# Kernel tuning notes

Measured on AMD Instinct MI355X. Metric: run time of the kernel, lower is better.

Reference implementation:

```python
import jax, jax.numpy as jnp
import numpy as np
from jax import lax

B = 512          # scoring batch size
NC = 10          # n_classes
N_LAB = 256      # int(B * plb), plb = 0.5 (labeled indices are the first N_LAB)
TOL = 1e-3       # gtg_t
MAX_ITER = 30    # gtg_i
INTERM = 128
CH = [64, 128, 256, 512]
SZ = [32, 16, 8, 4]
EMB = 512


def setup_inputs() -> dict:
    key = jax.random.key(0)
    ks = jax.random.split(key, 16)
    inp = {}
    for i, (c, s) in enumerate(zip(CH, SZ)):
        inp["feat%d" % i] = jax.random.normal(ks[i], (B, c, s, s), jnp.float32)
        inp["conv_w%d" % i] = jax.random.normal(ks[4 + i], (c, c, 3, 3), jnp.float32) * 0.05
        inp["conv_b%d" % i] = jnp.zeros((c,), jnp.float32)
        inp["bn_g%d" % i] = jnp.ones((c,), jnp.float32)
        inp["bn_b%d" % i] = jnp.zeros((c,), jnp.float32)
        inp["lin_w%d" % i] = jax.random.normal(ks[8 + i], (INTERM, c), jnp.float32) * 0.05
        inp["lin_b%d" % i] = jnp.zeros((INTERM,), jnp.float32)
    inp["fin_w"] = jax.random.normal(ks[12], (1, 4 * INTERM), jnp.float32) * 0.05
    inp["fin_b"] = jnp.zeros((1,), jnp.float32)
    inp["embedds"] = jax.random.normal(ks[13], (B, EMB), jnp.float32)
    inp["labels"] = jax.random.randint(ks[14], (B,), 0, NC)
    return inp


def _branch(x, cw, cb, g, b, lw, lb):
    # Conv3x3(same) -> BatchNorm (train mode, batch stats, eps=1e-5) -> ReLU -> GAP -> Linear -> ReLU
    y = lax.conv_general_dilated(x, cw, (1, 1), 'SAME',
                                 dimension_numbers=('NCHW', 'OIHW', 'NCHW')) + cb[None, :, None, None]
    m = y.mean(axis=(0, 2, 3), keepdims=True)
    v = ((y - m) ** 2).mean(axis=(0, 2, 3), keepdims=True)  # biased variance (train-mode BN)
    y = jax.nn.relu(g[None, :, None, None] * (y - m) * lax.rsqrt(v + 1e-5) + b[None, :, None, None])
    y = y.mean(axis=(2, 3))  # AvgPool2d(feature_size) == global average pool -> [B, C]
    return jax.nn.relu(y @ lw.T + lb)


def _gtg(E, labels):
    # get_A_e_d: pairwise euclidean distances clamped to [0.1, 1.0]
    sq = jnp.sum(E * E, axis=1)
    d2 = jnp.maximum(sq[:, None] + sq[None, :] - 2.0 * (E @ E.T), 0.0)
    A0 = jnp.clip(jnp.sqrt(d2), 0.1, 1.0)
    # rbf kernel: 7th nearest neighbor (ascending for 'e_d') gives per-sample sigma
    seventh = E[jnp.argsort(A0, axis=1)[:, 6]]
    sig = jnp.clip(jnp.sqrt(jnp.sum((E - seventh) ** 2, axis=1)), 0.1, 1.0)
    A = jnp.clip(jnp.exp(-(A0 ** 2) / (sig[:, None] * sig[None, :])), 0.0, 1.0)
    # threshold strategy 'mean' with AM_function == 'e_d': A = where(A > mean(A), 1, A)
    A = jnp.where(A > A.mean(), 1.0, A)
    # AM_strategy 'mixed' with 'e_d': flip only the labeled x labeled block
    A = A.at[:N_LAB, :N_LAB].set(1.0 - A[:N_LAB, :N_LAB])
    # get_X: one-hot for labeled (first N_LAB), uniform 1/NC for unlabeled
    X0 = jnp.concatenate([jax.nn.one_hot(labels[:N_LAB], NC, dtype=jnp.float32),
                          jnp.full((B - N_LAB, NC), 1.0 / NC, jnp.float32)], axis=0)
    hist0 = jnp.zeros((B, MAX_ITER), jnp.float32)

    def cond(c):
        return (c[3] > TOL) & (c[2] < MAX_ITER)

    def body(c):
        X, h, i, _ = c
        Xn = X * (A @ X)
        Xn = Xn / jnp.sum(Xn, axis=1, keepdims=True)
        ent = -jnp.sum(jnp.where(Xn > 0, Xn * jnp.log(Xn), 0.0), axis=1)
        h = lax.dynamic_update_slice(h, ent[:, None], (0, i))
        return (Xn, h, i + 1, jnp.linalg.norm(Xn - X))

    X, h, _, _ = lax.while_loop(cond, body, (X0, hist0, jnp.int32(0), jnp.float32(jnp.inf)))
    return h.mean(axis=1), X  # ent_strategy == 'mean'


def reference(feat0, feat1, feat2, feat3,
              conv_w0, conv_b0, bn_g0, bn_b0, lin_w0, lin_b0,
              conv_w1, conv_b1, bn_g1, bn_b1, lin_w1, lin_b1,
              conv_w2, conv_b2, bn_g2, bn_b2, lin_w2, lin_b2,
              conv_w3, conv_b3, bn_g3, bn_b3, lin_w3, lin_b3,
              fin_w, fin_b, embedds, labels):
    o0 = _branch(feat0, conv_w0, conv_b0, bn_g0, bn_b0, lin_w0, lin_b0)
    o1 = _branch(feat1, conv_w1, conv_b1, bn_g1, bn_b1, lin_w1, lin_b1)
    o2 = _branch(feat2, conv_w2, conv_b2, bn_g2, bn_b2, lin_w2, lin_b2)
    o3 = _branch(feat3, conv_w3, conv_b3, bn_g3, bn_b3, lin_w3, lin_b3)
    y_pred = (jnp.concatenate([o0, o1, o2, o3], axis=1) @ fin_w.T + fin_b)[:, 0]
    y_true, X = _gtg(embedds, labels)
    labeled_mask = jnp.arange(B) < N_LAB
    return (y_pred, y_true, X, labeled_mask)
```

## Files before the change

kernel.cpp:

```cpp
#include <hip/hip_runtime.h>
#include <hip/hip_bf16.h>
#include <math.h>

static constexpr int kNC = 10;
static constexpr int kNLab = 256;
static constexpr int kMaxIter = 30;

using short8 = __attribute__((ext_vector_type(8))) short;
using f32x4  = __attribute__((ext_vector_type(4))) float;

__device__ __forceinline__ unsigned short f2bf(float f) {
  unsigned int u = __float_as_uint(f);
  u += 0x7FFFu + ((u >> 16) & 1u);
  return (unsigned short)(u >> 16);
}
__device__ __forceinline__ float bf2f(unsigned short u) {
  return __uint_as_float(((unsigned int)u) << 16);
}

template <int C, int S>
__global__ __launch_bounds__(256) void xpack_kernel(const float* __restrict__ x,
                                                    unsigned short* __restrict__ xp) {
  __shared__ float t[C][S + 1];
  const int n = blockIdx.x / S, h = blockIdx.x % S;
  const float* src = x + (size_t)n * C * S * S;
  for (int e = threadIdx.x; e < C * S; e += 256) {
    int c = e / S, w = e % S;
    t[c][w] = src[((size_t)c * S + h) * S + w];
  }
  __syncthreads();
  unsigned short* dst = xp + ((size_t)(n * S + h) * S) * C;
  for (int e = threadIdx.x; e < C * S; e += 256) {
    int w = e / C, c = e % C;
    dst[(size_t)w * C + c] = f2bf(t[c][w]);
  }
}

template <int C>
__global__ void wpack_kernel(const float* __restrict__ w, unsigned short* __restrict__ wpk) {
  constexpr int CO16T = C / 16, CIK = C / 32;
  int idx = blockIdx.x * 256 + threadIdx.x;
  if (idx >= 9 * C * C) return;
  int e = idx & 7, l = (idx >> 3) & 63;
  int rest = idx >> 9;
  int co16 = rest % CO16T;
  int rest2 = rest / CO16T;
  int cik = rest2 % CIK, tap = rest2 / CIK;
  int co = co16 * 16 + (l & 15);
  int ci = cik * 32 + (l >> 4) * 8 + e;
  wpk[idx] = f2bf(w[((size_t)co * C + ci) * 9 + tap]);
}

template <int C, int S, int NI, int NR, int WV, int MODE>
__global__ __launch_bounds__(WV * 64)
void conv_mfma(const unsigned short* __restrict__ xp, const unsigned short* __restrict__ wpk,
               const float* __restrict__ bias, unsigned short* __restrict__ y,
               float* __restrict__ psum, float* __restrict__ psq, int npart, int partBase,
               const float* __restrict__ scale, const float* __restrict__ shift,
               float* __restrict__ pp, int pxGlobalBase) {
  constexpr int SS = S * S;
  constexpr int PXT = WV * 64;
  constexpr int HR = NR + 2, HC = S + 2;
  constexpr int CIK = C / 32, CO16T = C / 16;
  constexpr int UNITS = NI * HR * HC * 4;
  static_assert(NI * NR * S == PXT, "tile mismatch");
  __shared__ __align__(16) char xs[NI * HR * HC * 80];

  const int tid = threadIdx.x;
  const int wv = tid >> 6, l = tid & 63, l15 = l & 15, l4 = l >> 4;
  const int coblk = blockIdx.y;
  const int co_base = coblk * 64;
  const int pxb = blockIdx.x * PXT;
  const int n_t = pxb / SS;
  const int r0 = (pxb % SS) / S;

  int pxoff[4];
#pragma unroll
  for (int bf = 0; bf < 4; ++bf) {
    int pxloc = wv * 64 + bf * 16 + l15;
    int ii = pxloc / (NR * S);
    int rr = (pxloc % (NR * S)) / S;
    int cc = pxloc % S;
    pxoff[bf] = ((ii * HR + rr) * HC + cc) * 80 + l4 * 16;
  }

  f32x4 acc[4][4];
#pragma unroll
  for (int a = 0; a < 4; ++a)
#pragma unroll
    for (int b = 0; b < 4; ++b) acc[a][b] = (f32x4){0.f, 0.f, 0.f, 0.f};

  for (int cik = 0; cik < CIK; ++cik) {
    __syncthreads();
    for (int u = tid; u < UNITS; u += PXT) {
      int k16 = u & 3;
      int t = u >> 2;
      int hc = t % HC;
      int t2 = t / HC;
      int hr = t2 % HR;
      int ii = t2 / HR;
      int row = r0 + hr - 1, col = hc - 1;
      uint4 v = {0u, 0u, 0u, 0u};
      if (row >= 0 && row < S && col >= 0 && col < S)
        v = *(const uint4*)(xp + ((size_t)((n_t + ii) * S + row) * S + col) * C + cik * 32 + k16 * 8);
      *(uint4*)(xs + t * 80 + k16 * 16) = v;
    }
    __syncthreads();
#pragma unroll
    for (int tap = 0; tap < 9; ++tap) {
      const int tapoff = ((tap / 3) * HC + (tap % 3)) * 80;
      short8 wf[4], xf[4];
#pragma unroll
      for (int af = 0; af < 4; ++af)
        wf[af] = *(const short8*)(wpk + ((size_t)((tap * CIK + cik) * CO16T + coblk * 4 + af) * 64 + l) * 8);
#pragma unroll
      for (int bf = 0; bf < 4; ++bf)
        xf[bf] = *(const short8*)(xs + pxoff[bf] + tapoff);
#pragma unroll
      for (int af = 0; af < 4; ++af)
#pragma unroll
        for (int bf = 0; bf < 4; ++bf)
          acc[af][bf] = __builtin_amdgcn_mfma_f32_16x16x32_bf16(wf[af], xf[bf], acc[af][bf], 0, 0, 0);
    }
  }

#pragma unroll
  for (int af = 0; af < 4; ++af) {
    const int co0 = co_base + af * 16 + l4 * 4;
    float4 bv = *(const float4*)(bias + co0);
    float s[4] = {0.f, 0.f, 0.f, 0.f}, q[4] = {0.f, 0.f, 0.f, 0.f};
    float4 sc4, sh4;
    if (MODE == 2) {
      sc4 = *(const float4*)(scale + co0);
      sh4 = *(const float4*)(shift + co0);
    }
#pragma unroll
    for (int bf = 0; bf < 4; ++bf) {
      float o[4];
#pragma unroll
      for (int r = 0; r < 4; ++r) o[r] = acc[af][bf][r] + ((const float*)&bv)[r];
      if (MODE == 0) {
        ushort4 pk;
        pk.x = f2bf(o[0]); pk.y = f2bf(o[1]); pk.z = f2bf(o[2]); pk.w = f2bf(o[3]);
        size_t px = (size_t)(pxb + wv * 64 + bf * 16 + l15);
        *(ushort4*)(y + px * C + co0) = pk;
      }
      if (MODE == 2) {
#pragma unroll
        for (int r = 0; r < 4; ++r)
          s[r] += fmaxf(fmaf(((const float*)&sc4)[r], o[r], ((const float*)&sh4)[r]), 0.f);
      } else {
#pragma unroll
        for (int r = 0; r < 4; ++r) { s[r] += o[r]; q[r] += o[r] * o[r]; }
      }
    }
#pragma unroll
    for (int m = 1; m < 16; m <<= 1) {
#pragma unroll
      for (int r = 0; r < 4; ++r) {
        s[r] += __shfl_xor(s[r], m);
        if (MODE != 2) q[r] += __shfl_xor(q[r], m);
      }
    }
    if (l15 == 0) {
      if (MODE == 2) {
        int n = (pxGlobalBase + pxb) / SS;
        int qw = ((pxGlobalBase + pxb) % SS) / 64 + wv;
#pragma unroll
        for (int r = 0; r < 4; ++r)
          pp[((size_t)(n * C + co0 + r)) * 16 + qw] = s[r];
      } else {
        int part = partBase + blockIdx.x * WV + wv;
#pragma unroll
        for (int r = 0; r < 4; ++r) {
          psum[(size_t)(co0 + r) * npart + part] = s[r];
          psq[(size_t)(co0 + r) * npart + part] = q[r];
        }
      }
    }
  }
}

__global__ __launch_bounds__(256)
void stats2_kernel(const float* __restrict__ psum, const float* __restrict__ psq,
                   const float* __restrict__ g, const float* __restrict__ bb,
                   float* __restrict__ scale, float* __restrict__ shift,
                   int npart, float invN) {
  int c = blockIdx.x;
  __shared__ float rs[256], rq[256];
  float s = 0.f, q = 0.f;
  for (int p = threadIdx.x; p < npart; p += 256) {
    s += psum[(size_t)c * npart + p];
    q += psq[(size_t)c * npart + p];
  }
  rs[threadIdx.x] = s; rq[threadIdx.x] = q;
  __syncthreads();
  for (int st = 128; st; st >>= 1) {
    if (threadIdx.x < st) { rs[threadIdx.x] += rs[threadIdx.x + st]; rq[threadIdx.x] += rq[threadIdx.x + st]; }
    __syncthreads();
  }
  if (threadIdx.x == 0) {
    float m = rs[0] * invN;
    float v = rq[0] * invN - m * m;
    float sc = g[c] / sqrtf(v + 1e-5f);
    scale[c] = sc;
    shift[c] = bb[c] - m * sc;
  }
}

template <int C, int S>
__global__ __launch_bounds__(256)
void pool_nhwc(const unsigned short* __restrict__ y, const float* __restrict__ scale,
               const float* __restrict__ shift, float* __restrict__ pooled) {
  constexpr int SS = S * S;
  int n = blockIdx.x;
  const unsigned short* yr = y + (size_t)n * SS * C;
  if (C >= 256) {
    for (int co = threadIdx.x; co < C; co += 256) {
      float sc = scale[co], sh = shift[co], s = 0.f;
      for (int p = 0; p < SS; ++p) s += fmaxf(fmaf(sc, bf2f(yr[(size_t)p * C + co]), sh), 0.f);
      pooled[(size_t)n * C + co] = s * (1.f / SS);
    }
  } else {
    constexpr int G = 256 / C;
    int co = threadIdx.x % C;
    int sl = threadIdx.x / C;
    float sc = scale[co], sh = shift[co], s = 0.f;
    for (int p = sl; p < SS; p += G) s += fmaxf(fmaf(sc, bf2f(yr[(size_t)p * C + co]), sh), 0.f);
    __shared__ float red[256];
    red[threadIdx.x] = s;
    __syncthreads();
    if (threadIdx.x < C) {
      float t = 0.f;
      for (int gg = 0; gg < G; ++gg) t += red[gg * C + co];
      pooled[(size_t)n * C + co] = t * (1.f / SS);
    }
  }
}

__global__ void poolfin_kernel(const float* __restrict__ pp, float* __restrict__ pooled) {
  int i = blockIdx.x * 256 + threadIdx.x;
  if (i >= 512 * 64) return;
  float s = 0.f;
  for (int qn = 0; qn < 16; ++qn) s += pp[(size_t)i * 16 + qn];
  pooled[i] = s * (1.f / 1024.f);
}

__global__ void lin_kernel(const float* __restrict__ pooled, const float* __restrict__ lw,
                           const float* __restrict__ lb, float* __restrict__ oc,
                           int C, int brOff) {
  int idx = blockIdx.x * 256 + threadIdx.x;
  if (idx >= 512 * 128) return;
  int j = idx & 127, n = idx >> 7;
  const float4* pr = (const float4*)(pooled + (size_t)n * C);
  const float4* wr = (const float4*)(lw + (size_t)j * C);
  float s = 0.f;
  for (int t = 0; t < C / 4; ++t) {
    float4 a = pr[t], b = wr[t];
    s += a.x * b.x + a.y * b.y + a.z * b.z + a.w * b.w;
  }
  s += lb[j];
  oc[n * 512 + brOff + j] = fmaxf(s, 0.f);
}

__global__ void ypred_kernel(const float* __restrict__ oc, const float* __restrict__ fw,
                             const float* __restrict__ fb, float* __restrict__ out) {
  int wv = threadIdx.x >> 6, l = threadIdx.x & 63;
  int n = blockIdx.x * 4 + wv;
  float s = 0.f;
  for (int k = l; k < 512; k += 64) s += oc[n * 512 + k] * fw[k];
#pragma unroll
  for (int m = 32; m; m >>= 1) s += __shfl_down(s, m);
  if (l == 0) out[n] = s + fb[0];
}

__global__ void sqnorm_kernel(const float* __restrict__ E, float* __restrict__ sq) {
  int wv = threadIdx.x >> 6, l = threadIdx.x & 63;
  int n = blockIdx.x * 4 + wv;
  const float* row = E + (size_t)n * 512;
  float s = 0.f;
  for (int k = l; k < 512; k += 64) { float v = row[k]; s += v * v; }
#pragma unroll
  for (int m = 32; m; m >>= 1) s += __shfl_down(s, m);
  if (l == 0) sq[n] = s;
}

__global__ __launch_bounds__(256) void a0_kernel(const float* __restrict__ E,
                                                 const float* __restrict__ sq,
                                                 float* __restrict__ A0) {
  int bi = blockIdx.x / 32, bj = blockIdx.x % 32;
  int ti = threadIdx.x % 16, tj = threadIdx.x / 16;
  __shared__ float Ei[16][68], Ej[16][68];
  float acc = 0.f;
  for (int k0 = 0; k0 < 512; k0 += 64) {
    for (int e = threadIdx.x; e < 1024; e += 256) {
      int rr = e >> 6, cc = e & 63;
      Ei[rr][cc] = E[(size_t)(bi * 16 + rr) * 512 + k0 + cc];
      Ej[rr][cc] = E[(size_t)(bj * 16 + rr) * 512 + k0 + cc];
    }
    __syncthreads();
#pragma unroll 16
    for (int kk = 0; kk < 64; ++kk) acc = fmaf(Ei[tj][kk], Ej[ti][kk], acc);
    __syncthreads();
  }
  int i = bi * 16 + tj, j = bj * 16 + ti;
  float d2 = fmaxf(sq[i] + sq[j] - 2.f * acc, 0.f);
  A0[(size_t)i * 512 + j] = fminf(fmaxf(sqrtf(d2), 0.1f), 1.0f);
}

__global__ void seventh_kernel(const float* __restrict__ A0, int* __restrict__ idx7) {
  int i = blockIdx.x * 256 + threadIdx.x;
  if (i >= 512) return;
  float v[7]; int ix[7];
#pragma unroll
  for (int t = 0; t < 7; ++t) { v[t] = 3.4e38f; ix[t] = 0; }
  const float* row = A0 + (size_t)i * 512;
  for (int j = 0; j < 512; ++j) {
    float a = row[j];
    if (a < v[6]) {
      int pos = 6;
      while (pos > 0 && a < v[pos - 1]) { v[pos] = v[pos - 1]; ix[pos] = ix[pos - 1]; --pos; }
      v[pos] = a; ix[pos] = j;
    }
  }
  idx7[i] = ix[6];
}

__global__ void sig_kernel(const float* __restrict__ E, const int* __restrict__ idx7,
                           float* __restrict__ sig) {
  int wv = threadIdx.x >> 6, l = threadIdx.x & 63;
  int n = blockIdx.x * 4 + wv;
  const float* r1 = E + (size_t)n * 512;
  const float* r2 = E + (size_t)idx7[n] * 512;
  float s = 0.f;
  for (int k = l; k < 512; k += 64) { float d = r1[k] - r2[k]; s += d * d; }
#pragma unroll
  for (int m = 32; m; m >>= 1) s += __shfl_down(s, m);
  if (l == 0) sig[n] = fminf(fmaxf(sqrtf(s), 0.1f), 1.0f);
}

__global__ void aexp_kernel(const float* __restrict__ A0, const float* __restrict__ sig,
                            float* __restrict__ A, float* __restrict__ part) {
  int t = blockIdx.x * 256 + threadIdx.x;
  int base = t * 4;
  int i = base >> 9, j0 = base & 511;
  float si = sig[i];
  float4 a = *(const float4*)(A0 + base);
  float4 o;
  o.x = fminf(fmaxf(expf(-a.x * a.x / (si * sig[j0 + 0])), 0.f), 1.f);
  o.y = fminf(fmaxf(expf(-a.y * a.y / (si * sig[j0 + 1])), 0.f), 1.f);
  o.z = fminf(fmaxf(expf(-a.z * a.z / (si * sig[j0 + 2])), 0.f), 1.f);
  o.w = fminf(fmaxf(expf(-a.w * a.w / (si * sig[j0 + 3])), 0.f), 1.f);
  *(float4*)(A + base) = o;
  float lsum = o.x + o.y + o.z + o.w;
#pragma unroll
  for (int m = 32; m; m >>= 1) lsum += __shfl_down(lsum, m);
  __shared__ float sred[4];
  if ((threadIdx.x & 63) == 0) sred[threadIdx.x >> 6] = lsum;
  __syncthreads();
  if (threadIdx.x == 0) part[blockIdx.x] = sred[0] + sred[1] + sred[2] + sred[3];
}

__global__ void meanred_kernel(const float* __restrict__ part, float* __restrict__ meanA) {
  if (threadIdx.x == 0 && blockIdx.x == 0) {
    float s = 0.f;
    for (int p = 0; p < 256; ++p) s += part[p];
    meanA[0] = s * (1.0f / 262144.0f);
  }
}

__global__ void thresh_kernel(float* __restrict__ A, const float* __restrict__ meanA) {
  int t = blockIdx.x * 256 + threadIdx.x;
  int base = t * 4;
  int i = base >> 9, j0 = base & 511;
  float m = meanA[0];
  float4 v = *(const float4*)(A + base);
  v.x = v.x > m ? 1.f : v.x;
  v.y = v.y > m ? 1.f : v.y;
  v.z = v.z > m ? 1.f : v.z;
  v.w = v.w > m ? 1.f : v.w;
  if (i < kNLab && j0 < kNLab) {
    v.x = 1.f - v.x; v.y = 1.f - v.y; v.z = 1.f - v.z; v.w = 1.f - v.w;
  }
  *(float4*)(A + base) = v;
}

__global__ void init_kernel(const int* __restrict__ labels, float* __restrict__ X0,
                            float* __restrict__ hist) {
  int i = blockIdx.x * 256 + threadIdx.x;
  if (i < 512 * kMaxIter) hist[i] = 0.f;
  if (i < 512 * kNC) {
    int r = i / kNC, c = i % kNC;
    X0[i] = (r < kNLab) ? ((labels[r] == c) ? 1.f : 0.f) : 0.1f;
  }
}

__global__ __launch_bounds__(256)
void iter_kernel(const float* __restrict__ A, const float* __restrict__ Xin,
                 float* __restrict__ Xout, float* __restrict__ hist,
                 float* __restrict__ diffPart, int it) {
  bool active = true;
  if (it > 0) {
    float s = 0.f;
    for (int p = 0; p < 64; ++p) s += diffPart[(it - 1) * 64 + p];
    active = (sqrtf(s) > 0.001f);
  }
  __shared__ float dred[8];
  int i = blockIdx.x * 8 + (threadIdx.x >> 5);
  int l = threadIdx.x & 31;
  if (active) {
    float ax[kNC];
#pragma unroll
    for (int c = 0; c < kNC; ++c) ax[c] = 0.f;
    for (int jb = l; jb < 512; jb += 32) {
      float a = A[(size_t)i * 512 + jb];
      const float* xr = Xin + jb * kNC;
#pragma unroll
      for (int c = 0; c < kNC; ++c) ax[c] = fmaf(a, xr[c], ax[c]);
    }
#pragma unroll
    for (int c = 0; c < kNC; ++c)
      for (int m = 16; m; m >>= 1) ax[c] += __shfl_xor(ax[c], m, 32);
    if (l == 0) {
      float xn[kNC], s = 0.f;
#pragma unroll
      for (int c = 0; c < kNC; ++c) { xn[c] = Xin[i * kNC + c] * ax[c]; s += xn[c]; }
      float ent = 0.f, dp = 0.f;
#pragma unroll
      for (int c = 0; c < kNC; ++c) {
        float xv = xn[c] / s;
        if (xv > 0.f) ent -= xv * logf(xv);
        float d = xv - Xin[i * kNC + c];
        dp += d * d;
        Xout[i * kNC + c] = xv;
      }
      hist[i * kMaxIter + it] = ent;
      dred[threadIdx.x >> 5] = dp;
    }
    __syncthreads();
    if (threadIdx.x == 0) {
      float s2 = 0.f;
      for (int rr = 0; rr < 8; ++rr) s2 += dred[rr];
      diffPart[it * 64 + blockIdx.x] = s2;
    }
  } else {
    for (int e = threadIdx.x; e < 80; e += 256)
      Xout[blockIdx.x * 80 + e] = Xin[blockIdx.x * 80 + e];
    if (threadIdx.x == 0) diffPart[it * 64 + blockIdx.x] = 0.f;
  }
}

__global__ void final_kernel(const float* __restrict__ hist, const float* __restrict__ Xf,
                             float* __restrict__ out) {
  int i = blockIdx.x * 256 + threadIdx.x;
  if (i < 512) {
    float s = 0.f;
    for (int t = 0; t < kMaxIter; ++t) s += hist[i * kMaxIter + t];
    out[512 + i] = s * (1.0f / 30.0f);
    out[6144 + i] = (i < kNLab) ? 1.0f : 0.0f;
  }
  if (i < 512 * kNC) out[1024 + i] = Xf[i];
}

extern "C" void kernel_launch(void* const* d_in, const int* in_sizes, int n_in,
                              void* d_out, int out_size, void* d_ws, size_t ws_size,
                              hipStream_t stream) {
  (void)in_sizes; (void)n_in; (void)out_size; (void)ws_size;

  const float* feat[4]; const float* cw[4]; const float* cbp[4];
  const float* bg[4]; const float* bbp[4]; const float* lw[4]; const float* lbp[4];
  for (int b = 0; b < 4; ++b) {
    int base = b * 7;
    feat[b] = (const float*)d_in[base + 0];
    cw[b]  = (const float*)d_in[base + 1];
    cbp[b] = (const float*)d_in[base + 2];
    bg[b]  = (const float*)d_in[base + 3];
    bbp[b] = (const float*)d_in[base + 4];
    lw[b]  = (const float*)d_in[base + 5];
    lbp[b] = (const float*)d_in[base + 6];
  }
  const float* finw = (const float*)d_in[28];
  const float* finb = (const float*)d_in[29];
  const float* emb  = (const float*)d_in[30];
  const int* labels = (const int*)d_in[31];
  float* out = (float*)d_out;

  float* wsf = (float*)d_ws;
  unsigned short* xpad = (unsigned short*)wsf;
  unsigned short* yP   = (unsigned short*)(wsf + 4194304);
  unsigned short* wpk  = (unsigned short*)(wsf + 12582912);
  size_t off = 13762560;
  float* psum = wsf + off; off += 524288;
  float* psq  = wsf + off; off += 524288;
  float* pp   = wsf + off; off += 524288;
  float* scale = wsf + off; off += 512;
  float* shift = wsf + off; off += 512;
  float* pooled = wsf + off; off += 491520;
  float* oc = wsf + off; off += 262144;
  float* sq = wsf + off; off += 512;
  float* A0 = wsf + off; off += 262144;
  float* Am = wsf + off; off += 262144;
  float* sig = wsf + off; off += 512;
  int* idx7 = (int*)(wsf + off); off += 512;
  float* meanPart = wsf + off; off += 256;
  float* meanA = wsf + off; off += 4;
  float* X0 = wsf + off; off += 5120;
  float* X1 = wsf + off; off += 5120;
  float* hist = wsf + off; off += 15360;
  float* diffPart = wsf + off; off += 1920;

  wpack_kernel<128><<<(9 * 128 * 128 + 255) / 256, 256, 0, stream>>>(cw[1], wpk);
  for (int c = 0; c < 2; ++c) {
    xpack_kernel<128, 16><<<256 * 16, 256, 0, stream>>>(feat[1] + (size_t)c * 8388608, xpad);
    conv_mfma<128, 16, 1, 16, 4, 0><<<dim3(256, 2), 256, 0, stream>>>(
        xpad, wpk, cbp[1], yP + (size_t)c * 8388608, psum, psq, 2048, c * 1024,
        nullptr, nullptr, nullptr, 0);
  }
  stats2_kernel<<<128, 256, 0, stream>>>(psum, psq, bg[1], bbp[1], scale, shift, 2048, 1.f / 131072.f);
  pool_nhwc<128, 16><<<512, 256, 0, stream>>>(yP, scale, shift, pooled + 32768);
  lin_kernel<<<256, 256, 0, stream>>>(pooled + 32768, lw[1], lbp[1], oc, 128, 128);

  wpack_kernel<256><<<(9 * 256 * 256 + 255) / 256, 256, 0, stream>>>(cw[2], wpk);
  xpack_kernel<256, 8><<<512 * 8, 256, 0, stream>>>(feat[2], xpad);
  conv_mfma<256, 8, 4, 8, 4, 0><<<dim3(128, 4), 256, 0, stream>>>(
      xpad, wpk, cbp[2], yP, psum, psq, 512, 0, nullptr, nullptr, nullptr, 0);
  stats2_kernel<<<256, 256, 0, stream>>>(psum, psq, bg[2], bbp[2], scale, shift, 512, 1.f / 32768.f);
  pool_nhwc<256, 8><<<512, 256, 0, stream>>>(yP, scale, shift, pooled + 98304);
  lin_kernel<<<256, 256, 0, stream>>>(pooled + 98304, lw[2], lbp[2], oc, 256, 256);

  wpack_kernel<512><<<(9 * 512 * 512 + 255) / 256, 256, 0, stream>>>(cw[3], wpk);
  xpack_kernel<512, 4><<<512 * 4, 256, 0, stream>>>(feat[3], xpad);
  conv_mfma<512, 4, 8, 4, 2, 0><<<dim3(64, 8), 128, 0, stream>>>(
      xpad, wpk, cbp[3], yP, psum, psq, 128, 0, nullptr, nullptr, nullptr, 0);
  stats2_kernel<<<512, 256, 0, stream>>>(psum, psq, bg[3], bbp[3], scale, shift, 128, 1.f / 8192.f);
  pool_nhwc<512, 4><<<512, 256, 0, stream>>>(yP, scale, shift, pooled + 229376);
  lin_kernel<<<256, 256, 0, stream>>>(pooled + 229376, lw[3], lbp[3], oc, 512, 384);

  wpack_kernel<64><<<(9 * 64 * 64 + 255) / 256, 256, 0, stream>>>(cw[0], wpk);
  for (int c = 0; c < 4; ++c) {
    xpack_kernel<64, 32><<<128 * 32, 256, 0, stream>>>(feat[0] + (size_t)c * 8388608, xpad);
    conv_mfma<64, 32, 1, 8, 4, 1><<<dim3(512, 1), 256, 0, stream>>>(
        xpad, wpk, cbp[0], nullptr, psum, psq, 8192, c * 2048, nullptr, nullptr, nullptr, 0);
  }
  stats2_kernel<<<64, 256, 0, stream>>>(psum, psq, bg[0], bbp[0], scale, shift, 8192, 1.f / 524288.f);
  for (int c = 0; c < 4; ++c) {
    xpack_kernel<64, 32><<<128 * 32, 256, 0, stream>>>(feat[0] + (size_t)c * 8388608, xpad);
    conv_mfma<64, 32, 1, 8, 4, 2><<<dim3(512, 1), 256, 0, stream>>>(
        xpad, wpk, cbp[0], nullptr, nullptr, nullptr, 0, 0, scale, shift, pp, c * 131072);
  }
  poolfin_kernel<<<128, 256, 0, stream>>>(pp, pooled);
  lin_kernel<<<256, 256, 0, stream>>>(pooled, lw[0], lbp[0], oc, 64, 0);

  ypred_kernel<<<128, 256, 0, stream>>>(oc, finw, finb, out);
  sqnorm_kernel<<<128, 256, 0, stream>>>(emb, sq);
  a0_kernel<<<1024, 256, 0, stream>>>(emb, sq, A0);
  seventh_kernel<<<2, 256, 0, stream>>>(A0, idx7);
  sig_kernel<<<128, 256, 0, stream>>>(emb, idx7, sig);
  aexp_kernel<<<256, 256, 0, stream>>>(A0, sig, Am, meanPart);
  meanred_kernel<<<1, 64, 0, stream>>>(meanPart, meanA);
  thresh_kernel<<<256, 256, 0, stream>>>(Am, meanA);
  init_kernel<<<60, 256, 0, stream>>>(labels, X0, hist);
  float* xb[2] = {X0, X1};
  for (int it = 0; it < kMaxIter; ++it)
    iter_kernel<<<64, 256, 0, stream>>>(Am, xb[it & 1], xb[(it + 1) & 1], hist, diffPart, it);
  final_kernel<<<20, 256, 0, stream>>>(hist, X0, out);
}
```

Measured before the change: 1.138 ms.

## Merge weight packing, prefetch conv tiles, store branch-0 conv, persistent GTG loop

Packs all four conv weight sets in one kernel. Register-prefetches the next input-channel slice so global loads overlap MFMA work, and retunes the per-wave pixel tiling (BF) and grid shapes. When the workspace is large enough, branch 0 stores its conv output once instead of running the conv twice (stats pass, then normalize/pool pass). The 30 GTG iteration launches plus init and final become a single persistent kernel with an atomic grid barrier, which removes launch overhead and allows an early break. The grid barrier assumes all 64 blocks are co-resident, and the extra buffer raises workspace use.

```diff
diff --git a/kernel.cpp b/kernel.cpp
--- a/kernel.cpp
+++ b/kernel.cpp
@@ -36,22 +36,29 @@
   }
 }
 
-template <int C>
-__global__ void wpack_kernel(const float* __restrict__ w, unsigned short* __restrict__ wpk) {
-  constexpr int CO16T = C / 16, CIK = C / 32;
+__global__ void wpack_all(const float* __restrict__ w0, const float* __restrict__ w1,
+                          const float* __restrict__ w2, const float* __restrict__ w3,
+                          unsigned short* __restrict__ wpk) {
   int idx = blockIdx.x * 256 + threadIdx.x;
-  if (idx >= 9 * C * C) return;
-  int e = idx & 7, l = (idx >> 3) & 63;
-  int rest = idx >> 9;
+  if (idx >= 3133440) return;
+  const float* w; int C, off;
+  if (idx < 36864)        { w = w0; C = 64;  off = 0; }
+  else if (idx < 184320)  { w = w1; C = 128; off = 36864; }
+  else if (idx < 774144)  { w = w2; C = 256; off = 184320; }
+  else                    { w = w3; C = 512; off = 774144; }
+  int e = idx - off;
+  int CO16T = C / 16, CIK = C / 32;
+  int e8 = e & 7, l = (e >> 3) & 63;
+  int rest = e >> 9;
   int co16 = rest % CO16T;
   int rest2 = rest / CO16T;
   int cik = rest2 % CIK, tap = rest2 / CIK;
   int co = co16 * 16 + (l & 15);
-  int ci = cik * 32 + (l >> 4) * 8 + e;
+  int ci = cik * 32 + (l >> 4) * 8 + e8;
   wpk[idx] = f2bf(w[((size_t)co * C + ci) * 9 + tap]);
 }
 
-template <int C, int S, int NI, int NR, int WV, int MODE>
+template <int C, int S, int NI, int NR, int WV, int BF, int MODE>
 __global__ __launch_bounds__(WV * 64)
 void conv_mfma(const unsigned short* __restrict__ xp, const unsigned short* __restrict__ wpk,
                const float* __restrict__ bias, unsigned short* __restrict__ y,
@@ -59,67 +66,85 @@
                const float* __restrict__ scale, const float* __restrict__ shift,
                float* __restrict__ pp, int pxGlobalBase) {
   constexpr int SS = S * S;
-  constexpr int PXT = WV * 64;
+  constexpr int PXB = NI * NR * S;
+  constexpr int TPB = WV * 64;
   constexpr int HR = NR + 2, HC = S + 2;
   constexpr int CIK = C / 32, CO16T = C / 16;
   constexpr int UNITS = NI * HR * HC * 4;
-  static_assert(NI * NR * S == PXT, "tile mismatch");
+  constexpr int NU = (UNITS + TPB - 1) / TPB;
+  static_assert(WV * BF * 16 == PXB, "wave px mismatch");
+  static_assert(MODE != 2 || BF == 4, "MODE2 assumes 64px/wave");
   __shared__ __align__(16) char xs[NI * HR * HC * 80];
 
   const int tid = threadIdx.x;
   const int wv = tid >> 6, l = tid & 63, l15 = l & 15, l4 = l >> 4;
   const int coblk = blockIdx.y;
   const int co_base = coblk * 64;
-  const int pxb = blockIdx.x * PXT;
+  const int pxb = blockIdx.x * PXB;
   const int n_t = pxb / SS;
   const int r0 = (pxb % SS) / S;
 
-  int pxoff[4];
-#pragma unroll
-  for (int bf = 0; bf < 4; ++bf) {
-    int pxloc = wv * 64 + bf * 16 + l15;
+  int pxoff[BF];
+#pragma unroll
+  for (int bf = 0; bf < BF; ++bf) {
+    int pxloc = wv * (BF * 16) + bf * 16 + l15;
     int ii = pxloc / (NR * S);
     int rr = (pxloc % (NR * S)) / S;
     int cc = pxloc % S;
     pxoff[bf] = ((ii * HR + rr) * HC + cc) * 80 + l4 * 16;
   }
 
-  f32x4 acc[4][4];
+  f32x4 acc[4][BF];
 #pragma unroll
   for (int a = 0; a < 4; ++a)
 #pragma unroll
-    for (int b = 0; b < 4; ++b) acc[a][b] = (f32x4){0.f, 0.f, 0.f, 0.f};
-
+    for (int b = 0; b < BF; ++b) acc[a][b] = (f32x4){0.f, 0.f, 0.f, 0.f};
+
+  uint4 vreg[NU];
+  auto loadU = [&](int cik) {
+#pragma unroll
+    for (int k = 0; k < NU; ++k) {
+      int u = tid + k * TPB;
+      uint4 v = {0u, 0u, 0u, 0u};
+      if (u < UNITS) {
+        int k16 = u & 3;
+        int t = u >> 2;
+        int hc = t % HC;
+        int t2 = t / HC;
+        int hr = t2 % HR;
+        int ii = t2 / HR;
+        int row = r0 + hr - 1, col = hc - 1;
+        if (row >= 0 && row < S && col >= 0 && col < S)
+          v = *(const uint4*)(xp + ((size_t)((n_t + ii) * S + row) * S + col) * C + cik * 32 + k16 * 8);
+      }
+      vreg[k] = v;
+    }
+  };
+
+  loadU(0);
   for (int cik = 0; cik < CIK; ++cik) {
     __syncthreads();
-    for (int u = tid; u < UNITS; u += PXT) {
-      int k16 = u & 3;
-      int t = u >> 2;
-      int hc = t % HC;
-      int t2 = t / HC;
-      int hr = t2 % HR;
-      int ii = t2 / HR;
-      int row = r0 + hr - 1, col = hc - 1;
-      uint4 v = {0u, 0u, 0u, 0u};
-      if (row >= 0 && row < S && col >= 0 && col < S)
-        v = *(const uint4*)(xp + ((size_t)((n_t + ii) * S + row) * S + col) * C + cik * 32 + k16 * 8);
-      *(uint4*)(xs + t * 80 + k16 * 16) = v;
-    }
-    __syncthreads();
+#pragma unroll
+    for (int k = 0; k < NU; ++k) {
+      int u = tid + k * TPB;
+      if (u < UNITS) *(uint4*)(xs + (u >> 2) * 80 + (u & 3) * 16) = vreg[k];
+    }
+    __syncthreads();
+    if (cik + 1 < CIK) loadU(cik + 1);
 #pragma unroll
     for (int tap = 0; tap < 9; ++tap) {
       const int tapoff = ((tap / 3) * HC + (tap % 3)) * 80;
-      short8 wf[4], xf[4];
+      short8 wf[4], xf[BF];
 #pragma unroll
       for (int af = 0; af < 4; ++af)
         wf[af] = *(const short8*)(wpk + ((size_t)((tap * CIK + cik) * CO16T + coblk * 4 + af) * 64 + l) * 8);
 #pragma unroll
-      for (int bf = 0; bf < 4; ++bf)
+      for (int bf = 0; bf < BF; ++bf)
         xf[bf] = *(const short8*)(xs + pxoff[bf] + tapoff);
 #pragma unroll
       for (int af = 0; af < 4; ++af)
 #pragma unroll
-        for (int bf = 0; bf < 4; ++bf)
+        for (int bf = 0; bf < BF; ++bf)
           acc[af][bf] = __builtin_amdgcn_mfma_f32_16x16x32_bf16(wf[af], xf[bf], acc[af][bf], 0, 0, 0);
     }
   }
@@ -135,14 +160,14 @@
       sh4 = *(const float4*)(shift + co0);
     }
 #pragma unroll
-    for (int bf = 0; bf < 4; ++bf) {
+    for (int bf = 0; bf < BF; ++bf) {
       float o[4];
 #pragma unroll
       for (int r = 0; r < 4; ++r) o[r] = acc[af][bf][r] + ((const float*)&bv)[r];
       if (MODE == 0) {
         ushort4 pk;
         pk.x = f2bf(o[0]); pk.y = f2bf(o[1]); pk.z = f2bf(o[2]); pk.w = f2bf(o[3]);
-        size_t px = (size_t)(pxb + wv * 64 + bf * 16 + l15);
+        size_t px = (size_t)(pxb + wv * (BF * 16) + bf * 16 + l15);
         *(ushort4*)(y + px * C + co0) = pk;
       }
       if (MODE == 2) {
@@ -385,87 +410,108 @@
   *(float4*)(A + base) = v;
 }
 
-__global__ void init_kernel(const int* __restrict__ labels, float* __restrict__ X0,
-                            float* __restrict__ hist) {
-  int i = blockIdx.x * 256 + threadIdx.x;
-  if (i < 512 * kMaxIter) hist[i] = 0.f;
-  if (i < 512 * kNC) {
-    int r = i / kNC, c = i % kNC;
-    X0[i] = (r < kNLab) ? ((labels[r] == c) ? 1.f : 0.f) : 0.1f;
-  }
+__device__ __forceinline__ void gridbar(int* cnt, int* sense, int ph) {
+  __syncthreads();
+  if (threadIdx.x == 0) {
+    __threadfence();
+    if (__hip_atomic_fetch_add(cnt, 1, __ATOMIC_ACQ_REL, __HIP_MEMORY_SCOPE_AGENT) == 63) {
+      __hip_atomic_store(cnt, 0, __ATOMIC_RELAXED, __HIP_MEMORY_SCOPE_AGENT);
+      __hip_atomic_store(sense, ph, __ATOMIC_RELEASE, __HIP_MEMORY_SCOPE_AGENT);
+    } else {
+      while (__hip_atomic_load(sense, __ATOMIC_ACQUIRE, __HIP_MEMORY_SCOPE_AGENT) < ph)
+        __builtin_amdgcn_s_sleep(2);
+    }
+  }
+  __syncthreads();
 }
 
 __global__ __launch_bounds__(256)
-void iter_kernel(const float* __restrict__ A, const float* __restrict__ Xin,
-                 float* __restrict__ Xout, float* __restrict__ hist,
-                 float* __restrict__ diffPart, int it) {
-  bool active = true;
-  if (it > 0) {
+void gtg_iters(const float* __restrict__ A, const int* __restrict__ labels,
+               float* __restrict__ Xa, float* __restrict__ Xb,
+               float* __restrict__ hist, float* __restrict__ diffPart,
+               float* __restrict__ out, int* __restrict__ bar) {
+  constexpr int NB = 64;
+  const int b = blockIdx.x, tid = threadIdx.x;
+  const int wv = tid >> 6, l = tid & 63;
+  __shared__ float Xs[512 * kNC];
+  __shared__ float red[4];
+  int* cnt = bar; int* sense = bar + 1;
+  int ph = 0;
+
+  for (int e = tid; e < 8 * kNC; e += 256) {
+    int r = b * 8 + e / kNC, c = e % kNC;
+    Xa[r * kNC + c] = (r < kNLab) ? ((labels[r] == c) ? 1.f : 0.f) : 0.1f;
+  }
+  for (int e = tid; e < 8 * kMaxIter; e += 256)
+    hist[(size_t)(b * 8 + e / kMaxIter) * kMaxIter + e % kMaxIter] = 0.f;
+  gridbar(cnt, sense, ++ph);
+
+  float* Xin = Xa;
+  float* Xout = Xb;
+  int it = 0;
+  for (; it < kMaxIter; ++it) {
+    if (it > 0) {
+      float s = 0.f;
+      for (int p = 0; p < NB; ++p) s += diffPart[(it - 1) * NB + p];
+      if (sqrtf(s) <= 0.001f) break;
+    }
+    for (int e = tid; e < 512 * kNC; e += 256) Xs[e] = Xin[e];
+    __syncthreads();
+    float dpw = 0.f;
+    for (int rr = 0; rr < 2; ++rr) {
+      int i = b * 8 + wv * 2 + rr;
+      const float* Ar = A + (size_t)i * 512;
+      float ax[kNC];
+#pragma unroll
+      for (int c = 0; c < kNC; ++c) ax[c] = 0.f;
+      for (int j = l; j < 512; j += 64) {
+        float a = Ar[j];
+        const float* xr = Xs + j * kNC;
+#pragma unroll
+        for (int c = 0; c < kNC; ++c) ax[c] = fmaf(a, xr[c], ax[c]);
+      }
+#pragma unroll
+      for (int c = 0; c < kNC; ++c)
+#pragma unroll
+        for (int m = 32; m; m >>= 1) ax[c] += __shfl_xor(ax[c], m);
+      if (l == 0) {
+        float xn[kNC], ssum = 0.f;
+#pragma unroll
+        for (int c = 0; c < kNC; ++c) { xn[c] = Xs[i * kNC + c] * ax[c]; ssum += xn[c]; }
+        float ent = 0.f, dp = 0.f;
+#pragma unroll
+        for (int c = 0; c < kNC; ++c) {
+          float xv = xn[c] / ssum;
+          if (xv > 0.f) ent -= xv * logf(xv);
+          float d = xv - Xs[i * kNC + c];
+          dp += d * d;
+          Xout[i * kNC + c] = xv;
+        }
+        hist[(size_t)i * kMaxIter + it] = ent;
+        dpw += dp;
+      }
+    }
+    if (l == 0) red[wv] = dpw;
+    __syncthreads();
+    if (tid == 0) diffPart[it * NB + b] = red[0] + red[1] + red[2] + red[3];
+    gridbar(cnt, sense, ++ph);
+    float* tmp = Xin; Xin = Xout; Xout = tmp;
+  }
+
+  if (tid < 8) {
+    int i = b * 8 + tid;
     float s = 0.f;
-    for (int p = 0; p < 64; ++p) s += diffPart[(it - 1) * 64 + p];
-    active = (sqrtf(s) > 0.001f);
-  }
-  __shared__ float dred[8];
-  int i = blockIdx.x * 8 + (threadIdx.x >> 5);
-  int l = threadIdx.x & 31;
-  if (active) {
-    float ax[kNC];
-#pragma unroll
-    for (int c = 0; c < kNC; ++c) ax[c] = 0.f;
-    for (int jb = l; jb < 512; jb += 32) {
-      float a = A[(size_t)i * 512 + jb];
-      const float* xr = Xin + jb * kNC;
-#pragma unroll
-      for (int c = 0; c < kNC; ++c) ax[c] = fmaf(a, xr[c], ax[c]);
-    }
-#pragma unroll
-    for (int c = 0; c < kNC; ++c)
-      for (int m = 16; m; m >>= 1) ax[c] += __shfl_xor(ax[c], m, 32);
-    if (l == 0) {
-      float xn[kNC], s = 0.f;
-#pragma unroll
-      for (int c = 0; c < kNC; ++c) { xn[c] = Xin[i * kNC + c] * ax[c]; s += xn[c]; }
-      float ent = 0.f, dp = 0.f;
-#pragma unroll
-      for (int c = 0; c < kNC; ++c) {
-        float xv = xn[c] / s;
-        if (xv > 0.f) ent -= xv * logf(xv);
-        float d = xv - Xin[i * kNC + c];
-        dp += d * d;
-        Xout[i * kNC + c] = xv;
-      }
-      hist[i * kMaxIter + it] = ent;
-      dred[threadIdx.x >> 5] = dp;
-    }
-    __syncthreads();
-    if (threadIdx.x == 0) {
-      float s2 = 0.f;
-      for (int rr = 0; rr < 8; ++rr) s2 += dred[rr];
-      diffPart[it * 64 + blockIdx.x] = s2;
-    }
-  } else {
-    for (int e = threadIdx.x; e < 80; e += 256)
-      Xout[blockIdx.x * 80 + e] = Xin[blockIdx.x * 80 + e];
-    if (threadIdx.x == 0) diffPart[it * 64 + blockIdx.x] = 0.f;
-  }
-}
-
-__global__ void final_kernel(const float* __restrict__ hist, const float* __restrict__ Xf,
-                             float* __restrict__ out) {
-  int i = blockIdx.x * 256 + threadIdx.x;
-  if (i < 512) {
-    float s = 0.f;
-    for (int t = 0; t < kMaxIter; ++t) s += hist[i * kMaxIter + t];
+    for (int t = 0; t < kMaxIter; ++t) s += hist[(size_t)i * kMaxIter + t];
     out[512 + i] = s * (1.0f / 30.0f);
     out[6144 + i] = (i < kNLab) ? 1.0f : 0.0f;
   }
-  if (i < 512 * kNC) out[1024 + i] = Xf[i];
+  for (int e = tid; e < 80; e += 256) out[1024 + b * 80 + e] = Xin[b * 80 + e];
 }
 
 extern "C" void kernel_launch(void* const* d_in, const int* in_sizes, int n_in,
                               void* d_out, int out_size, void* d_ws, size_t ws_size,
                               hipStream_t stream) {
-  (void)in_sizes; (void)n_in; (void)out_size; (void)ws_size;
+  (void)in_sizes; (void)n_in; (void)out_size;
 
   const float* feat[4]; const float* cw[4]; const float* cbp[4];
   const float* bg[4]; const float* bbp[4]; const float* lw[4]; const float* lbp[4];
@@ -489,7 +535,7 @@
   unsigned short* xpad = (unsigned short*)wsf;
   unsigned short* yP   = (unsigned short*)(wsf + 4194304);
   unsigned short* wpk  = (unsigned short*)(wsf + 12582912);
-  size_t off = 13762560;
+  size_t off = 14149632;
   float* psum = wsf + off; off += 524288;
   float* psq  = wsf + off; off += 524288;
   float* pp   = wsf + off; off += 524288;
@@ -508,47 +554,62 @@
   float* X1 = wsf + off; off += 5120;
   float* hist = wsf + off; off += 15360;
   float* diffPart = wsf + off; off += 1920;
-
-  wpack_kernel<128><<<(9 * 128 * 128 + 255) / 256, 256, 0, stream>>>(cw[1], wpk);
+  int* bar = (int*)(wsf + off); off += 4;
+  size_t yb0_off = off;
+  unsigned short* yB0 = (unsigned short*)(wsf + yb0_off);
+  const bool bigB0 = ws_size >= (yb0_off + 16777216) * sizeof(float);
+
+  unsigned short* wpkB[4] = {wpk, wpk + 36864, wpk + 184320, wpk + 774144};
+
+  wpack_all<<<(3133440 + 255) / 256, 256, 0, stream>>>(cw[0], cw[1], cw[2], cw[3], wpk);
+
   for (int c = 0; c < 2; ++c) {
     xpack_kernel<128, 16><<<256 * 16, 256, 0, stream>>>(feat[1] + (size_t)c * 8388608, xpad);
-    conv_mfma<128, 16, 1, 16, 4, 0><<<dim3(256, 2), 256, 0, stream>>>(
-        xpad, wpk, cbp[1], yP + (size_t)c * 8388608, psum, psq, 2048, c * 1024,
+    conv_mfma<128, 16, 1, 8, 4, 2, 0><<<dim3(512, 2), 256, 0, stream>>>(
+        xpad, wpkB[1], cbp[1], yP + (size_t)c * 8388608, psum, psq, 4096, c * 2048,
         nullptr, nullptr, nullptr, 0);
   }
-  stats2_kernel<<<128, 256, 0, stream>>>(psum, psq, bg[1], bbp[1], scale, shift, 2048, 1.f / 131072.f);
+  stats2_kernel<<<128, 256, 0, stream>>>(psum, psq, bg[1], bbp[1], scale, shift, 4096, 1.f / 131072.f);
   pool_nhwc<128, 16><<<512, 256, 0, stream>>>(yP, scale, shift, pooled + 32768);
   lin_kernel<<<256, 256, 0, stream>>>(pooled + 32768, lw[1], lbp[1], oc, 128, 128);
 
-  wpack_kernel<256><<<(9 * 256 * 256 + 255) / 256, 256, 0, stream>>>(cw[2], wpk);
   xpack_kernel<256, 8><<<512 * 8, 256, 0, stream>>>(feat[2], xpad);
-  conv_mfma<256, 8, 4, 8, 4, 0><<<dim3(128, 4), 256, 0, stream>>>(
-      xpad, wpk, cbp[2], yP, psum, psq, 512, 0, nullptr, nullptr, nullptr, 0);
-  stats2_kernel<<<256, 256, 0, stream>>>(psum, psq, bg[2], bbp[2], scale, shift, 512, 1.f / 32768.f);
+  conv_mfma<256, 8, 2, 8, 4, 2, 0><<<dim3(256, 4), 256, 0, stream>>>(
+      xpad, wpkB[2], cbp[2], yP, psum, psq, 1024, 0, nullptr, nullptr, nullptr, 0);
+  stats2_kernel<<<256, 256, 0, stream>>>(psum, psq, bg[2], bbp[2], scale, shift, 1024, 1.f / 32768.f);
   pool_nhwc<256, 8><<<512, 256, 0, stream>>>(yP, scale, shift, pooled + 98304);
   lin_kernel<<<256, 256, 0, stream>>>(pooled + 98304, lw[2], lbp[2], oc, 256, 256);
 
-  wpack_kernel<512><<<(9 * 512 * 512 + 255) / 256, 256, 0, stream>>>(cw[3], wpk);
   xpack_kernel<512, 4><<<512 * 4, 256, 0, stream>>>(feat[3], xpad);
-  conv_mfma<512, 4, 8, 4, 2, 0><<<dim3(64, 8), 128, 0, stream>>>(
-      xpad, wpk, cbp[3], yP, psum, psq, 128, 0, nullptr, nullptr, nullptr, 0);
-  stats2_kernel<<<512, 256, 0, stream>>>(psum, psq, bg[3], bbp[3], scale, shift, 128, 1.f / 8192.f);
+  conv_mfma<512, 4, 8, 4, 4, 2, 0><<<dim3(64, 8), 256, 0, stream>>>(
+      xpad, wpkB[3], cbp[3], yP, psum, psq, 256, 0, nullptr, nullptr, nullptr, 0);
+  stats2_kernel<<<512, 256, 0, stream>>>(psum, psq, bg[3], bbp[3], scale, shift, 256, 1.f / 8192.f);
   pool_nhwc<512, 4><<<512, 256, 0, stream>>>(yP, scale, shift, pooled + 229376);
   lin_kernel<<<256, 256, 0, stream>>>(pooled + 229376, lw[3], lbp[3], oc, 512, 384);
 
-  wpack_kernel<64><<<(9 * 64 * 64 + 255) / 256, 256, 0, stream>>>(cw[0], wpk);
-  for (int c = 0; c < 4; ++c) {
-    xpack_kernel<64, 32><<<128 * 32, 256, 0, stream>>>(feat[0] + (size_t)c * 8388608, xpad);
-    conv_mfma<64, 32, 1, 8, 4, 1><<<dim3(512, 1), 256, 0, stream>>>(
-        xpad, wpk, cbp[0], nullptr, psum, psq, 8192, c * 2048, nullptr, nullptr, nullptr, 0);
-  }
-  stats2_kernel<<<64, 256, 0, stream>>>(psum, psq, bg[0], bbp[0], scale, shift, 8192, 1.f / 524288.f);
-  for (int c = 0; c < 4; ++c) {
-    xpack_kernel<64, 32><<<128 * 32, 256, 0, stream>>>(feat[0] + (size_t)c * 8388608, xpad);
-    conv_mfma<64, 32, 1, 8, 4, 2><<<dim3(512, 1), 256, 0, stream>>>(
-        xpad, wpk, cbp[0], nullptr, nullptr, nullptr, 0, 0, scale, shift, pp, c * 131072);
-  }
-  poolfin_kernel<<<128, 256, 0, stream>>>(pp, pooled);
+  if (bigB0) {
+    for (int c = 0; c < 4; ++c) {
+      xpack_kernel<64, 32><<<128 * 32, 256, 0, stream>>>(feat[0] + (size_t)c * 8388608, xpad);
+      conv_mfma<64, 32, 1, 8, 4, 4, 0><<<dim3(512, 1), 256, 0, stream>>>(
+          xpad, wpkB[0], cbp[0], yB0 + (size_t)c * 8388608, psum, psq, 8192, c * 2048,
+          nullptr, nullptr, nullptr, 0);
+    }
+    stats2_kernel<<<64, 256, 0, stream>>>(psum, psq, bg[0], bbp[0], scale, shift, 8192, 1.f / 524288.f);
+    pool_nhwc<64, 32><<<512, 256, 0, stream>>>(yB0, scale, shift, pooled);
+  } else {
+    for (int c = 0; c < 4; ++c) {
+      xpack_kernel<64, 32><<<128 * 32, 256, 0, stream>>>(feat[0] + (size_t)c * 8388608, xpad);
+      conv_mfma<64, 32, 1, 8, 4, 4, 1><<<dim3(512, 1), 256, 0, stream>>>(
+          xpad, wpkB[0], cbp[0], nullptr, psum, psq, 8192, c * 2048, nullptr, nullptr, nullptr, 0);
+    }
+    stats2_kernel<<<64, 256, 0, stream>>>(psum, psq, bg[0], bbp[0], scale, shift, 8192, 1.f / 524288.f);
+    for (int c = 0; c < 4; ++c) {
+      xpack_kernel<64, 32><<<128 * 32, 256, 0, stream>>>(feat[0] + (size_t)c * 8388608, xpad);
+      conv_mfma<64, 32, 1, 8, 4, 4, 2><<<dim3(512, 1), 256, 0, stream>>>(
+          xpad, wpkB[0], cbp[0], nullptr, nullptr, nullptr, 0, 0, scale, shift, pp, c * 131072);
+    }
+    poolfin_kernel<<<128, 256, 0, stream>>>(pp, pooled);
+  }
   lin_kernel<<<256, 256, 0, stream>>>(pooled, lw[0], lbp[0], oc, 64, 0);
 
   ypred_kernel<<<128, 256, 0, stream>>>(oc, finw, finb, out);
@@ -559,9 +620,7 @@
   aexp_kernel<<<256, 256, 0, stream>>>(A0, sig, Am, meanPart);
   meanred_kernel<<<1, 64, 0, stream>>>(meanPart, meanA);
   thresh_kernel<<<256, 256, 0, stream>>>(Am, meanA);
-  init_kernel<<<60, 256, 0, stream>>>(labels, X0, hist);
-  float* xb[2] = {X0, X1};
-  for (int it = 0; it < kMaxIter; ++it)
-    iter_kernel<<<64, 256, 0, stream>>>(Am, xb[it & 1], xb[(it + 1) & 1], hist, diffPart, it);
-  final_kernel<<<20, 256, 0, stream>>>(hist, X0, out);
-}
+
+  hipMemsetAsync(bar, 0, 8, stream);
+  gtg_iters<<<64, 256, 0, stream>>>(Am, labels, X0, X1, hist, diffPart, out, bar);
+}
```

Result: faster. 1.016 ms (-10.8%).
